# Performance work log

Measured on AMD Instinct MI355X. Metric: run time of the kernel, lower is better.

Reference implementation:

```python
import jax, jax.numpy as jnp
import numpy as np

D = 1024
HID = D // 2          # 512
HLEN = 15
IN_DIM = 4
B, N = 32, 512
EPS = 1e-5


def setup_inputs() -> dict:
    key = jax.random.key(0)
    ks = jax.random.split(key, 16)
    inp = {
        "tokens": jax.random.normal(ks[0], (B, N, D), dtype=jnp.float32),
        "history_traj": jax.random.normal(ks[1], (B, N, HLEN, IN_DIM), dtype=jnp.float32),
        "history_abs": jax.random.normal(ks[2], (B, N, 2), dtype=jnp.float32),
        "ego_speed": jax.random.uniform(ks[3], (B,), dtype=jnp.float32),
        "gps_confidence": jax.random.uniform(ks[4], (B,), dtype=jnp.float32),
        # LSTM params (PyTorch layout: gates stacked i,f,g,o along dim 0)
        "W_ih": jax.random.normal(ks[5], (4 * HID, IN_DIM), dtype=jnp.float32) * (1.0 / np.sqrt(IN_DIM)),
        "W_hh": jax.random.normal(ks[6], (4 * HID, HID), dtype=jnp.float32) * (1.0 / np.sqrt(HID)),
        "b_ih": jnp.zeros((4 * HID,), dtype=jnp.float32),
        "b_hh": jnp.zeros((4 * HID,), dtype=jnp.float32),
        "W_rel": jax.random.normal(ks[7], (D, HID), dtype=jnp.float32) * (0.1 / np.sqrt(HID)),
        "W_abs": jax.random.normal(ks[8], (D, 2), dtype=jnp.float32) * 0.1,
        "W_g1": jax.random.normal(ks[9], (16, 2), dtype=jnp.float32) * 0.5,
        "b_g1": jnp.zeros((16,), dtype=jnp.float32),
        "W_g2": jax.random.normal(ks[10], (1, 16), dtype=jnp.float32) * 0.25,
        "b_g2": jnp.zeros((1,), dtype=jnp.float32),
        "gamma": jnp.ones((D,), dtype=jnp.float32),
        "beta": jnp.zeros((D,), dtype=jnp.float32),
    }
    return inp


def _lstm_final_hidden(x, W_ih, W_hh, b_ih, b_hh):
    """x: (BN, H, in) -> final hidden state (BN, HID). PyTorch gate order i,f,g,o."""
    BN = x.shape[0]
    # precompute input contribution for all steps: (H, BN, 4*HID)
    xg = jnp.einsum('bhi,gi->hbg', x, W_ih) + (b_ih + b_hh)

    def step(carry, xg_t):
        h, c = carry
        gates = xg_t + h @ W_hh.T  # (BN, 4*HID)
        i, f, g, o = jnp.split(gates, 4, axis=-1)
        i = jax.nn.sigmoid(i)
        f = jax.nn.sigmoid(f)
        g = jnp.tanh(g)
        o = jax.nn.sigmoid(o)
        c = f * c + i * g
        h = o * jnp.tanh(c)
        return (h, c), None

    h0 = jnp.zeros((BN, HID), dtype=x.dtype)
    c0 = jnp.zeros((BN, HID), dtype=x.dtype)
    (h, _), _ = jax.lax.scan(step, (h0, c0), xg)
    return h


def reference(tokens, history_traj, history_abs, ego_speed, gps_confidence,
              W_ih, W_hh, b_ih, b_hh, W_rel, W_abs, W_g1, b_g1, W_g2, b_g2,
              gamma, beta):
    Bv, Nv, Dv = tokens.shape
    Hv = history_traj.shape[2]
    traj_flat = history_traj.reshape(Bv * Nv, Hv, -1)
    h_n = _lstm_final_hidden(traj_flat, W_ih, W_hh, b_ih, b_hh)  # (B*N, HID)
    h_rel = (h_n @ W_rel.T).reshape(Bv, Nv, Dv)                  # (B, N, D)
    h_abs = history_abs @ W_abs.T                                # (B, N, D)
    conf = jnp.stack([ego_speed, gps_confidence], axis=-1)       # (B, 2)
    gate = jax.nn.relu(conf @ W_g1.T + b_g1) @ W_g2.T + b_g2     # (B, 1)
    alpha = jax.nn.sigmoid(gate)[:, None, :]                     # (B, 1, 1)
    h_fused = alpha * h_rel + (1.0 - alpha) * h_abs
    x = tokens + h_fused
    mu = jnp.mean(x, axis=-1, keepdims=True)
    var = jnp.mean(jnp.square(x - mu), axis=-1, keepdims=True)
    return (x - mu) * jax.lax.rsqrt(var + EPS) * gamma + beta
```

## Files before the change

kernel.cpp:

```cpp
#include <hip/hip_runtime.h>
#include <hip/hip_bf16.h>
#include <math.h>

#define BB 32
#define NN 512
#define BN 16384
#define DD 1024
#define HID 512
#define G4 2048
#define HLEN 15
#define IND 4
#define EPS 1e-5f

typedef __bf16 v8bf __attribute__((ext_vector_type(8)));
typedef float  v4f  __attribute__((ext_vector_type(4)));

__device__ __forceinline__ void async_copy16(const __bf16* gsrc, __bf16* ldst) {
    __builtin_amdgcn_global_load_lds(
        (const __attribute__((address_space(1))) void*)gsrc,
        (__attribute__((address_space(3))) void*)ldst, 16, 0, 0);
}

#define VMCNTI(n) asm volatile("s_waitcnt vmcnt(" #n ")" ::: "memory")
#define VMCNT4 VMCNTI(4)
#define VMCNT0 VMCNTI(0)
#define LGKM0  asm volatile("s_waitcnt lgkmcnt(0)" ::: "memory")
#define MEMFENCE asm volatile("" ::: "memory")

#define LOG2E 1.44269504f
__device__ __forceinline__ float sigmf(float x) {
    return __builtin_amdgcn_rcpf(1.0f + __builtin_amdgcn_exp2f(-LOG2E * x));
}
__device__ __forceinline__ float tanh_fast(float x) {
    return 1.0f - 2.0f * __builtin_amdgcn_rcpf(1.0f + __builtin_amdgcn_exp2f(2.0f * LOG2E * x));
}

__global__ void convert_w(const float* __restrict__ Whh, const float* __restrict__ Wrel,
                          const float* __restrict__ Wih, const float* __restrict__ bih,
                          const float* __restrict__ bhh,
                          __bf16* __restrict__ whh_b, __bf16* __restrict__ wrel_b,
                          float* __restrict__ wih_i, float* __restrict__ bsum) {
    int i = blockIdx.x * 256 + threadIdx.x;
    if (i < G4 * HID) whh_b[i] = (__bf16)Whh[i];
    if (i < DD * HID) wrel_b[i] = (__bf16)Wrel[i];
    if (i < G4) {
        int uu = i >> 2, gi = i & 3;
        int src = gi * HID + uu;
        wih_i[i * 4 + 0] = Wih[src * 4 + 0];
        wih_i[i * 4 + 1] = Wih[src * 4 + 1];
        wih_i[i * 4 + 2] = Wih[src * 4 + 2];
        wih_i[i * 4 + 3] = Wih[src * 4 + 3];
        bsum[i] = bih[src] + bhh[src];
    }
}

__global__ void alpha_kernel(const float* __restrict__ es, const float* __restrict__ gc,
                             const float* __restrict__ W_g1, const float* __restrict__ b_g1,
                             const float* __restrict__ W_g2, const float* __restrict__ b_g2,
                             float* __restrict__ alpha) {
    int b = threadIdx.x;
    if (b >= BB) return;
    float c0 = es[b], c1 = gc[b];
    float acc = b_g2[0];
    for (int k = 0; k < 16; ++k) {
        float hk = c0 * W_g1[k * 2] + c1 * W_g1[k * 2 + 1] + b_g1[k];
        hk = fmaxf(hk, 0.0f);
        acc += hk * W_g2[k];
    }
    alpha[b] = 1.0f / (1.0f + expf(-acc));
}

__global__ __launch_bounds__(256) void lstm_cell0(const float* __restrict__ traj,
                                                  const float* __restrict__ wih_i,
                                                  const float* __restrict__ bsum,
                                                  float* __restrict__ c,
                                                  __bf16* __restrict__ h) {
    int idx = blockIdx.x * 256 + threadIdx.x;
    int row = idx >> 9;
    float4 x = *(const float4*)(traj + (size_t)row * (HLEN * IND));
    int u = idx & 511;
    float g[4];
    #pragma unroll
    for (int gi = 0; gi < 4; ++gi) {
        int j = u * 4 + gi;
        float4 w = *(const float4*)(wih_i + (size_t)j * 4);
        g[gi] = bsum[j] + w.x * x.x + w.y * x.y + w.z * x.z + w.w * x.w;
    }
    float ig = sigmf(g[0]);
    float gg = tanh_fast(g[2]);
    float og = sigmf(g[3]);
    float cn = ig * gg;
    c[idx] = cn;
    h[idx] = (__bf16)(og * tanh_fast(cn));
}


__device__ __forceinline__ void bar_acq() {
    __builtin_amdgcn_s_barrier();
    LGKM0;
    __builtin_amdgcn_sched_barrier(0);
}
__device__ __forceinline__ void bar_rel() {
    __builtin_amdgcn_s_barrier();
    MEMFENCE;
}

template<int IG, int GH, bool RA, bool RB>
__device__ __forceinline__ void phase_read(const __bf16* smb, int wave_m, int wn,
                                           int mrow, int pcs,
                                           v8bf (&ar)[4][2], v8bf (&br)[2][2][2]) {
    if (RA) {
        #pragma unroll
        for (int ii = 0; ii < 4; ++ii)
            #pragma unroll
            for (int ks = 0; ks < 2; ++ks)
                ar[ii][ks] = *(const v8bf*)(smb +
                    (wave_m * 128 + IG * 64 + ii * 16 + mrow) * 64 + ks * 32 + pcs);
    }
    if (RB) {
        #pragma unroll
        for (int g2 = 0; g2 < 2; ++g2)
            #pragma unroll
            for (int ks = 0; ks < 2; ++ks)
                br[GH][g2][ks] = *(const v8bf*)(smb + 16384 +
                    ((GH * 2 + g2) * 64 + wn * 16 + mrow) * 64 + ks * 32 + pcs);
    }
}

template<int IG, int GH>
__device__ __forceinline__ void phase_mfma(v8bf (&ar)[4][2], v8bf (&br)[2][2][2],
                                           v4f (&acc)[8][4]) {
    __builtin_amdgcn_s_setprio(1);
    #pragma unroll
    for (int ii = 0; ii < 4; ++ii)
        #pragma unroll
        for (int g2 = 0; g2 < 2; ++g2)
            #pragma unroll
            for (int ks = 0; ks < 2; ++ks)
                acc[IG * 4 + ii][GH * 2 + g2] = __builtin_amdgcn_mfma_f32_16x16x32_bf16(
                    ar[ii][ks], br[GH][g2][ks], acc[IG * 4 + ii][GH * 2 + g2], 0, 0, 0);
    __builtin_amdgcn_s_setprio(0);
}

__global__ __launch_bounds__(512, 2) void gemm_lstm(const __bf16* __restrict__ A,
                                                    const __bf16* __restrict__ Bm,
                                                    const float* __restrict__ traj,
                                                    const float* __restrict__ wih_i,
                                                    const float* __restrict__ bsum,
                                                    float* __restrict__ c,
                                                    __bf16* __restrict__ h_out,
                                                    int t) {
    __shared__ __bf16 sm[2][32768];

    const int tid    = threadIdx.x;
    const int lane   = tid & 63;
    const int wave   = tid >> 6;
    const int wave_m = wave & 1;
    const int wn     = wave >> 1;
    const int bm     = blockIdx.x;
    const int ub     = blockIdx.y;

    const int mrow = lane & 15;
    const int pcs  = (((lane >> 4) ^ ((mrow >> 2) & 3)) << 3);

    const __bf16* pa[4];
    const __bf16* pb[4];
    #pragma unroll
    for (int s = 0; s < 4; ++s) {
        const int ca = tid + s * 512;
        const int r  = ca >> 3, p = ca & 7;
        const int sl = p >> 2, l2 = (p & 3) ^ ((r >> 2) & 3);
        pa[s] = A + (size_t)(bm * 256 + r) * HID + sl * 32 + l2 * 8;
        const int g = r >> 6, ul = r & 63;
        pb[s] = Bm + (size_t)(g * HID + ub * 64 + ul) * HID + sl * 32 + l2 * 8;
    }
    const int wb = wave * 512;

    #define STAGE_A(buf, kt) do {                                        \
        async_copy16(pa[0] + (kt) * 64, &sm[buf][wb]);                   \
        async_copy16(pa[1] + (kt) * 64, &sm[buf][wb + 4096]);            \
        async_copy16(pa[2] + (kt) * 64, &sm[buf][wb + 8192]);            \
        async_copy16(pa[3] + (kt) * 64, &sm[buf][wb + 12288]); } while (0)
    #define STAGE_BLO(buf, kt) do {                                      \
        async_copy16(pb[0] + (kt) * 64, &sm[buf][16384 + wb]);           \
        async_copy16(pb[1] + (kt) * 64, &sm[buf][16384 + wb + 4096]); } while (0)
    #define STAGE_BHI(buf, kt) do {                                      \
        async_copy16(pb[2] + (kt) * 64, &sm[buf][16384 + wb + 8192]);    \
        async_copy16(pb[3] + (kt) * 64, &sm[buf][16384 + wb + 12288]); } while (0)

    v4f  acc[8][4] = {};
    v8bf ar[4][2];
    v8bf br[2][2][2];

    STAGE_A(0, 0); STAGE_BLO(0, 0); STAGE_BHI(0, 0);
    VMCNTI(2);
    __builtin_amdgcn_s_barrier();
    MEMFENCE;

    #pragma unroll
    for (int kt = 0; kt < 7; ++kt) {
        const int cb = kt & 1, nb = cb ^ 1;
        const __bf16* smb = &sm[cb][0];
        phase_read<0, 0, true, true>(smb, wave_m, wn, mrow, pcs, ar, br);
        if (nb) { STAGE_A(1, kt + 1); } else { STAGE_A(0, kt + 1); }
        bar_acq();  phase_mfma<0, 0>(ar, br, acc);  bar_rel();
        phase_read<1, 0, true, false>(smb, wave_m, wn, mrow, pcs, ar, br);
        if (nb) { STAGE_BLO(1, kt + 1); } else { STAGE_BLO(0, kt + 1); }
        VMCNTI(6);
        bar_acq();  phase_mfma<1, 0>(ar, br, acc);  bar_rel();
        phase_read<1, 1, false, true>(smb, wave_m, wn, mrow, pcs, ar, br);
        if (nb) { STAGE_BHI(1, kt + 1); } else { STAGE_BHI(0, kt + 1); }
        bar_acq();  phase_mfma<1, 1>(ar, br, acc);  bar_rel();
        phase_read<0, 1, true, false>(smb, wave_m, wn, mrow, pcs, ar, br);
        VMCNTI(2);
        bar_acq();  phase_mfma<0, 1>(ar, br, acc);  bar_rel();
    }

    VMCNT0;
    __builtin_amdgcn_s_barrier();
    MEMFENCE;
    {
        const __bf16* smb = &sm[1][0];
        phase_read<0, 0, true, true >(smb, wave_m, wn, mrow, pcs, ar, br);
        LGKM0; __builtin_amdgcn_sched_barrier(0);  phase_mfma<0, 0>(ar, br, acc);
        phase_read<1, 0, true, false>(smb, wave_m, wn, mrow, pcs, ar, br);
        LGKM0; __builtin_amdgcn_sched_barrier(0);  phase_mfma<1, 0>(ar, br, acc);
        phase_read<1, 1, false, true>(smb, wave_m, wn, mrow, pcs, ar, br);
        LGKM0; __builtin_amdgcn_sched_barrier(0);  phase_mfma<1, 1>(ar, br, acc);
        phase_read<0, 1, true, false>(smb, wave_m, wn, mrow, pcs, ar, br);
        LGKM0; __builtin_amdgcn_sched_barrier(0);  phase_mfma<0, 1>(ar, br, acc);
    }
    #undef STAGE_A
    #undef STAGE_BLO
    #undef STAGE_BHI

    const int u_glob = ub * 64 + wn * 16 + mrow;
    const int crow4  = (lane >> 4) * 4;
    float wv[4][4], bs4[4];
    #pragma unroll
    for (int gi = 0; gi < 4; ++gi) {
        float4 wp = *(const float4*)(wih_i + (size_t)(u_glob * 4 + gi) * 4);
        wv[gi][0] = wp.x; wv[gi][1] = wp.y; wv[gi][2] = wp.z; wv[gi][3] = wp.w;
        bs4[gi] = bsum[u_glob * 4 + gi];
    }
    #pragma unroll
    for (int i = 0; i < 8; ++i) {
        const int growb = bm * 256 + wave_m * 128 + (i >> 2) * 64 + (i & 3) * 16 + crow4;
        #pragma unroll
        for (int r = 0; r < 4; ++r) {
            const int grow = growb + r;
            const float4 x = *(const float4*)(traj + (size_t)grow * (HLEN * IND) + t * IND);
            float g[4];
            #pragma unroll
            for (int gi = 0; gi < 4; ++gi)
                g[gi] = acc[i][gi][r] + bs4[gi]
                      + wv[gi][0] * x.x + wv[gi][1] * x.y + wv[gi][2] * x.z + wv[gi][3] * x.w;
            float ig = sigmf(g[0]);
            float fg = sigmf(g[1]);
            float gg = tanh_fast(g[2]);
            float og = sigmf(g[3]);
            size_t ci = (size_t)grow * HID + u_glob;
            float cn = fg * c[ci] + ig * gg;
            c[ci] = cn;
            h_out[ci] = (__bf16)(og * tanh_fast(cn));
        }
    }
}

__global__ __launch_bounds__(256) void gemm_proj(const __bf16* __restrict__ A,
                                                 const __bf16* __restrict__ Bm,
                                                 __bf16* __restrict__ Cout) {
    __shared__ __bf16 sA[3][128][32];
    __shared__ __bf16 sB[3][128][32];
    const int K = HID, Nn = DD;
    const int tid  = threadIdx.x;
    const int lane = tid & 63;
    const int wave = tid >> 6;
    const int wm = (wave & 1) * 64;
    const int wn = (wave >> 1) * 64;
    const int bm = blockIdx.x;
    const int bn = blockIdx.y;

    v4f acc[4][4] = {};

    const int srow   = tid >> 2;
    const int schunk = (tid & 3) ^ ((srow >> 1) & 3);

    const __bf16* gA = A  + (size_t)(bm * 128 + srow) * K + schunk * 8;
    const __bf16* gB = Bm + (size_t)(bn * 128 + srow) * K + schunk * 8;
    __bf16* lA = &sA[0][0][0] + wave * 512;
    __bf16* lB = &sB[0][0][0] + wave * 512;

    const int mrow = lane & 15;
    const int pc   = ((lane >> 4) ^ ((mrow >> 1) & 3)) * 8;

    #define STAGE(buf, kt)                                        \
        do {                                                      \
            const __bf16* pA_ = gA + (kt) * 32;                   \
            const __bf16* pB_ = gB + (kt) * 32;                   \
            __bf16* dA_ = lA + (buf) * 4096;                      \
            __bf16* dB_ = lB + (buf) * 4096;                      \
            async_copy16(pA_,          dA_);                      \
            async_copy16(pA_ + 64 * K, dA_ + 2048);               \
            async_copy16(pB_,          dB_);                      \
            async_copy16(pB_ + 64 * K, dB_ + 2048);               \
        } while (0)

    STAGE(0, 0);
    STAGE(1, 1);
    #pragma unroll
    for (int k = 0; k < 16; ++k) {
        if (k < 15) { VMCNT4; } else { VMCNT0; }
        __builtin_amdgcn_s_barrier();
        MEMFENCE;
        if (k + 2 < 16) STAGE((k + 2) % 3, k + 2);
        const int cur = k % 3;
        v8bf af[4], bfr[4];
        #pragma unroll
        for (int i = 0; i < 4; ++i) af[i]  = *(v8bf*)&sA[cur][wm + i * 16 + mrow][pc];
        #pragma unroll
        for (int j = 0; j < 4; ++j) bfr[j] = *(v8bf*)&sB[cur][wn + j * 16 + mrow][pc];
        #pragma unroll
        for (int i = 0; i < 4; ++i)
            #pragma unroll
            for (int j = 0; j < 4; ++j)
                acc[i][j] = __builtin_amdgcn_mfma_f32_16x16x32_bf16(af[i], bfr[j], acc[i][j], 0, 0, 0);
    }
    #undef STAGE

    const int ccol  = lane & 15;
    const int crow4 = (lane >> 4) * 4;
    #pragma unroll
    for (int i = 0; i < 4; ++i)
        #pragma unroll
        for (int j = 0; j < 4; ++j) {
            int gm = bm * 128 + wm + i * 16 + crow4;
            int gn = bn * 128 + wn + j * 16 + ccol;
            #pragma unroll
            for (int r = 0; r < 4; ++r)
                Cout[(size_t)(gm + r) * Nn + gn] = (__bf16)acc[i][j][r];
        }
}

__global__ __launch_bounds__(256) void fuse_ln(const float* __restrict__ tokens,
                                               const __bf16* __restrict__ hrel,
                                               const float* __restrict__ habs_in,
                                               const float* __restrict__ W_abs,
                                               const float* __restrict__ alpha,
                                               const float* __restrict__ gamma,
                                               const float* __restrict__ beta,
                                               float* __restrict__ out) {
    const int row = blockIdx.x;
    const int b   = row >> 9;
    const float al = alpha[b];
    const float a0 = habs_in[(size_t)row * 2];
    const float a1 = habs_in[(size_t)row * 2 + 1];
    const int tid  = threadIdx.x;
    const int lane = tid & 63;
    const int wave = tid >> 6;

    __shared__ float red[4];

    float x[4];
    float s = 0.0f;
    #pragma unroll
    for (int q = 0; q < 4; ++q) {
        int dcol = tid + q * 256;
        float habs = a0 * W_abs[dcol * 2] + a1 * W_abs[dcol * 2 + 1];
        float v = tokens[(size_t)row * DD + dcol]
                + al * (float)hrel[(size_t)row * DD + dcol]
                + (1.0f - al) * habs;
        x[q] = v;
        s += v;
    }
    #pragma unroll
    for (int off = 32; off > 0; off >>= 1) s += __shfl_down(s, off);
    if (lane == 0) red[wave] = s;
    __syncthreads();
    float mu = (red[0] + red[1] + red[2] + red[3]) * (1.0f / DD);

    float vs = 0.0f;
    #pragma unroll
    for (int q = 0; q < 4; ++q) {
        float d = x[q] - mu;
        vs += d * d;
    }
    #pragma unroll
    for (int off = 32; off > 0; off >>= 1) vs += __shfl_down(vs, off);
    __syncthreads();
    if (lane == 0) red[wave] = vs;
    __syncthreads();
    float var = (red[0] + red[1] + red[2] + red[3]) * (1.0f / DD);
    float rstd = rsqrtf(var + EPS);

    #pragma unroll
    for (int q = 0; q < 4; ++q) {
        int dcol = tid + q * 256;
        out[(size_t)row * DD + dcol] = (x[q] - mu) * rstd * gamma[dcol] + beta[dcol];
    }
}

extern "C" void kernel_launch(void* const* d_in, const int* in_sizes, int n_in,
                              void* d_out, int out_size, void* d_ws, size_t ws_size,
                              hipStream_t stream) {
    const float* tokens   = (const float*)d_in[0];
    const float* traj     = (const float*)d_in[1];
    const float* habs     = (const float*)d_in[2];
    const float* espeed   = (const float*)d_in[3];
    const float* gconf    = (const float*)d_in[4];
    const float* W_ih     = (const float*)d_in[5];
    const float* W_hh     = (const float*)d_in[6];
    const float* b_ih     = (const float*)d_in[7];
    const float* b_hh     = (const float*)d_in[8];
    const float* W_rel    = (const float*)d_in[9];
    const float* W_abs    = (const float*)d_in[10];
    const float* W_g1     = (const float*)d_in[11];
    const float* b_g1     = (const float*)d_in[12];
    const float* W_g2     = (const float*)d_in[13];
    const float* b_g2     = (const float*)d_in[14];
    const float* gamma    = (const float*)d_in[15];
    const float* beta     = (const float*)d_in[16];
    float* out = (float*)d_out;

    char* ws = (char*)d_ws;
    size_t off = 0;
    __bf16* whh_b  = (__bf16*)(ws + off); off += (size_t)G4 * HID * 2;
    __bf16* wrel_b = (__bf16*)(ws + off); off += (size_t)DD * HID * 2;
    float*  wih_i  = (float*)(ws + off);  off += (size_t)G4 * 4 * 4;
    float*  bsum   = (float*)(ws + off);  off += (size_t)G4 * 4;
    __bf16* h0     = (__bf16*)(ws + off); off += (size_t)BN * HID * 2;
    __bf16* h1     = (__bf16*)(ws + off); off += (size_t)BN * HID * 2;
    float*  c      = (float*)(ws + off);  off += (size_t)BN * HID * 4;
    __bf16* hrel   = (__bf16*)(ws + off); off += (size_t)BN * DD * 2;
    float*  alpha  = (float*)(ws + off);  off += 256;

    convert_w<<<(G4 * HID + 255) / 256, 256, 0, stream>>>(W_hh, W_rel, W_ih, b_ih, b_hh,
                                                          whh_b, wrel_b, wih_i, bsum);
    alpha_kernel<<<1, 64, 0, stream>>>(espeed, gconf, W_g1, b_g1, W_g2, b_g2, alpha);
    lstm_cell0<<<(BN * HID) / 256, 256, 0, stream>>>(traj, wih_i, bsum, c, h0);

    __bf16* hbuf[2] = {h0, h1};
    for (int t = 1; t < HLEN; ++t) {
        const __bf16* hin = hbuf[(t + 1) & 1];
        __bf16* hout = hbuf[t & 1];
        gemm_lstm<<<dim3(BN / 256, HID / 64), 512, 0, stream>>>(hin, whh_b, traj, wih_i, bsum,
                                                                c, hout, t);
    }
    gemm_proj<<<dim3(BN / 128, DD / 128), 256, 0, stream>>>(h0, wrel_b, hrel);
    fuse_ln<<<BN, 256, 0, stream>>>(tokens, hrel, habs, W_abs, alpha, gamma, beta, out);
}
```

Before: 1.057 ms.

## Reuse 256x256 pipelined GEMM body for projection and widen LDS XOR swizzle

Moves the 256-tile, 8-wave, double-buffered phased MFMA GEMM body into a shared macro and uses it for the output projection as well, replacing the smaller 128x128 three-stage kernel. It also changes the LDS swizzle from a 2-bit to a 3-bit XOR across the 64-element row, aiming to cut LDS bank conflicts in both GEMMs. The larger projection tile improves operand reuse but leaves only 256 blocks, and the swizzle change has to stay consistent between the staging addresses and the fragment reads.

Result: faster. 868.3 us (-17.9%).

```diff
diff --git a/kernel.cpp b/kernel.cpp
--- a/kernel.cpp
+++ b/kernel.cpp
@@ -22,7 +22,6 @@
 }
 
 #define VMCNTI(n) asm volatile("s_waitcnt vmcnt(" #n ")" ::: "memory")
-#define VMCNT4 VMCNTI(4)
 #define VMCNT0 VMCNTI(0)
 #define LGKM0  asm volatile("s_waitcnt lgkmcnt(0)" ::: "memory")
 #define MEMFENCE asm volatile("" ::: "memory")
@@ -115,7 +114,7 @@
             #pragma unroll
             for (int ks = 0; ks < 2; ++ks)
                 ar[ii][ks] = *(const v8bf*)(smb +
-                    (wave_m * 128 + IG * 64 + ii * 16 + mrow) * 64 + ks * 32 + pcs);
+                    (wave_m * 128 + IG * 64 + ii * 16 + mrow) * 64 + ((ks * 32) ^ pcs));
     }
     if (RB) {
         #pragma unroll
@@ -123,7 +122,7 @@
             #pragma unroll
             for (int ks = 0; ks < 2; ++ks)
                 br[GH][g2][ks] = *(const v8bf*)(smb + 16384 +
-                    ((GH * 2 + g2) * 64 + wn * 16 + mrow) * 64 + ks * 32 + pcs);
+                    ((GH * 2 + g2) * 64 + wn * 16 + mrow) * 64 + ((ks * 32) ^ pcs));
     }
 }
 
@@ -141,6 +140,59 @@
                     ar[ii][ks], br[GH][g2][ks], acc[IG * 4 + ii][GH * 2 + g2], 0, 0, 0);
     __builtin_amdgcn_s_setprio(0);
 }
+
+#define STAGE_A(buf, kt) do {                                        \
+    async_copy16(pa[0] + (kt) * 64, &sm[buf][wb]);                   \
+    async_copy16(pa[1] + (kt) * 64, &sm[buf][wb + 4096]);            \
+    async_copy16(pa[2] + (kt) * 64, &sm[buf][wb + 8192]);            \
+    async_copy16(pa[3] + (kt) * 64, &sm[buf][wb + 12288]); } while (0)
+#define STAGE_BLO(buf, kt) do {                                      \
+    async_copy16(pb[0] + (kt) * 64, &sm[buf][16384 + wb]);           \
+    async_copy16(pb[1] + (kt) * 64, &sm[buf][16384 + wb + 4096]); } while (0)
+#define STAGE_BHI(buf, kt) do {                                      \
+    async_copy16(pb[2] + (kt) * 64, &sm[buf][16384 + wb + 8192]);    \
+    async_copy16(pb[3] + (kt) * 64, &sm[buf][16384 + wb + 12288]); } while (0)
+
+#define GEMM256_BODY                                                               \
+    v4f  acc[8][4] = {};                                                           \
+    v8bf ar[4][2];                                                                 \
+    v8bf br[2][2][2];                                                              \
+    STAGE_A(0, 0); STAGE_BLO(0, 0); STAGE_BHI(0, 0);                               \
+    VMCNTI(2);                                                                     \
+    __builtin_amdgcn_s_barrier();                                                  \
+    MEMFENCE;                                                                      \
+    _Pragma("unroll")                                                              \
+    for (int kt = 0; kt < 7; ++kt) {                                               \
+        const int nb = (kt & 1) ^ 1;                                               \
+        const __bf16* smb = &sm[kt & 1][0];                                        \
+        phase_read<0, 0, true, true>(smb, wave_m, wn, mrow, pcs, ar, br);          \
+        if (nb) { STAGE_A(1, kt + 1); } else { STAGE_A(0, kt + 1); }               \
+        bar_acq();  phase_mfma<0, 0>(ar, br, acc);  bar_rel();                     \
+        phase_read<1, 0, true, false>(smb, wave_m, wn, mrow, pcs, ar, br);         \
+        if (nb) { STAGE_BLO(1, kt + 1); } else { STAGE_BLO(0, kt + 1); }           \
+        VMCNTI(6);                                                                 \
+        bar_acq();  phase_mfma<1, 0>(ar, br, acc);  bar_rel();                     \
+        phase_read<1, 1, false, true>(smb, wave_m, wn, mrow, pcs, ar, br);         \
+        if (nb) { STAGE_BHI(1, kt + 1); } else { STAGE_BHI(0, kt + 1); }           \
+        bar_acq();  phase_mfma<1, 1>(ar, br, acc);  bar_rel();                     \
+        phase_read<0, 1, true, false>(smb, wave_m, wn, mrow, pcs, ar, br);         \
+        VMCNTI(2);                                                                 \
+        bar_acq();  phase_mfma<0, 1>(ar, br, acc);  bar_rel();                     \
+    }                                                                              \
+    VMCNT0;                                                                        \
+    __builtin_amdgcn_s_barrier();                                                  \
+    MEMFENCE;                                                                      \
+    {                                                                              \
+        const __bf16* smb = &sm[1][0];                                             \
+        phase_read<0, 0, true, true >(smb, wave_m, wn, mrow, pcs, ar, br);         \
+        LGKM0; __builtin_amdgcn_sched_barrier(0);  phase_mfma<0, 0>(ar, br, acc);  \
+        phase_read<1, 0, true, false>(smb, wave_m, wn, mrow, pcs, ar, br);         \
+        LGKM0; __builtin_amdgcn_sched_barrier(0);  phase_mfma<1, 0>(ar, br, acc);  \
+        phase_read<1, 1, false, true>(smb, wave_m, wn, mrow, pcs, ar, br);         \
+        LGKM0; __builtin_amdgcn_sched_barrier(0);  phase_mfma<1, 1>(ar, br, acc);  \
+        phase_read<0, 1, true, false>(smb, wave_m, wn, mrow, pcs, ar, br);         \
+        LGKM0; __builtin_amdgcn_sched_barrier(0);  phase_mfma<0, 1>(ar, br, acc);  \
+    }
 
 __global__ __launch_bounds__(512, 2) void gemm_lstm(const __bf16* __restrict__ A,
                                                     const __bf16* __restrict__ Bm,
@@ -161,78 +213,22 @@
     const int ub     = blockIdx.y;
 
     const int mrow = lane & 15;
-    const int pcs  = (((lane >> 4) ^ ((mrow >> 2) & 3)) << 3);
+    const int pcs  = (((lane >> 4) ^ (mrow & 7)) << 3);
 
     const __bf16* pa[4];
     const __bf16* pb[4];
     #pragma unroll
     for (int s = 0; s < 4; ++s) {
         const int ca = tid + s * 512;
-        const int r  = ca >> 3, p = ca & 7;
-        const int sl = p >> 2, l2 = (p & 3) ^ ((r >> 2) & 3);
-        pa[s] = A + (size_t)(bm * 256 + r) * HID + sl * 32 + l2 * 8;
+        const int r  = ca >> 3;
+        const int l  = (ca & 7) ^ (r & 7);
+        pa[s] = A + (size_t)(bm * 256 + r) * HID + l * 8;
         const int g = r >> 6, ul = r & 63;
-        pb[s] = Bm + (size_t)(g * HID + ub * 64 + ul) * HID + sl * 32 + l2 * 8;
+        pb[s] = Bm + (size_t)(g * HID + ub * 64 + ul) * HID + l * 8;
     }
     const int wb = wave * 512;
 
-    #define STAGE_A(buf, kt) do {                                        \
-        async_copy16(pa[0] + (kt) * 64, &sm[buf][wb]);                   \
-        async_copy16(pa[1] + (kt) * 64, &sm[buf][wb + 4096]);            \
-        async_copy16(pa[2] + (kt) * 64, &sm[buf][wb + 8192]);            \
-        async_copy16(pa[3] + (kt) * 64, &sm[buf][wb + 12288]); } while (0)
-    #define STAGE_BLO(buf, kt) do {                                      \
-        async_copy16(pb[0] + (kt) * 64, &sm[buf][16384 + wb]);           \
-        async_copy16(pb[1] + (kt) * 64, &sm[buf][16384 + wb + 4096]); } while (0)
-    #define STAGE_BHI(buf, kt) do {                                      \
-        async_copy16(pb[2] + (kt) * 64, &sm[buf][16384 + wb + 8192]);    \
-        async_copy16(pb[3] + (kt) * 64, &sm[buf][16384 + wb + 12288]); } while (0)
-
-    v4f  acc[8][4] = {};
-    v8bf ar[4][2];
-    v8bf br[2][2][2];
-
-    STAGE_A(0, 0); STAGE_BLO(0, 0); STAGE_BHI(0, 0);
-    VMCNTI(2);
-    __builtin_amdgcn_s_barrier();
-    MEMFENCE;
-
-    #pragma unroll
-    for (int kt = 0; kt < 7; ++kt) {
-        const int cb = kt & 1, nb = cb ^ 1;
-        const __bf16* smb = &sm[cb][0];
-        phase_read<0, 0, true, true>(smb, wave_m, wn, mrow, pcs, ar, br);
-        if (nb) { STAGE_A(1, kt + 1); } else { STAGE_A(0, kt + 1); }
-        bar_acq();  phase_mfma<0, 0>(ar, br, acc);  bar_rel();
-        phase_read<1, 0, true, false>(smb, wave_m, wn, mrow, pcs, ar, br);
-        if (nb) { STAGE_BLO(1, kt + 1); } else { STAGE_BLO(0, kt + 1); }
-        VMCNTI(6);
-        bar_acq();  phase_mfma<1, 0>(ar, br, acc);  bar_rel();
-        phase_read<1, 1, false, true>(smb, wave_m, wn, mrow, pcs, ar, br);
-        if (nb) { STAGE_BHI(1, kt + 1); } else { STAGE_BHI(0, kt + 1); }
-        bar_acq();  phase_mfma<1, 1>(ar, br, acc);  bar_rel();
-        phase_read<0, 1, true, false>(smb, wave_m, wn, mrow, pcs, ar, br);
-        VMCNTI(2);
-        bar_acq();  phase_mfma<0, 1>(ar, br, acc);  bar_rel();
-    }
-
-    VMCNT0;
-    __builtin_amdgcn_s_barrier();
-    MEMFENCE;
-    {
-        const __bf16* smb = &sm[1][0];
-        phase_read<0, 0, true, true >(smb, wave_m, wn, mrow, pcs, ar, br);
-        LGKM0; __builtin_amdgcn_sched_barrier(0);  phase_mfma<0, 0>(ar, br, acc);
-        phase_read<1, 0, true, false>(smb, wave_m, wn, mrow, pcs, ar, br);
-        LGKM0; __builtin_amdgcn_sched_barrier(0);  phase_mfma<1, 0>(ar, br, acc);
-        phase_read<1, 1, false, true>(smb, wave_m, wn, mrow, pcs, ar, br);
-        LGKM0; __builtin_amdgcn_sched_barrier(0);  phase_mfma<1, 1>(ar, br, acc);
-        phase_read<0, 1, true, false>(smb, wave_m, wn, mrow, pcs, ar, br);
-        LGKM0; __builtin_amdgcn_sched_barrier(0);  phase_mfma<0, 1>(ar, br, acc);
-    }
-    #undef STAGE_A
-    #undef STAGE_BLO
-    #undef STAGE_BHI
+    GEMM256_BODY
 
     const int u_glob = ub * 64 + wn * 16 + mrow;
     const int crow4  = (lane >> 4) * 4;
@@ -267,79 +263,48 @@
     }
 }
 
-__global__ __launch_bounds__(256) void gemm_proj(const __bf16* __restrict__ A,
-                                                 const __bf16* __restrict__ Bm,
-                                                 __bf16* __restrict__ Cout) {
-    __shared__ __bf16 sA[3][128][32];
-    __shared__ __bf16 sB[3][128][32];
-    const int K = HID, Nn = DD;
-    const int tid  = threadIdx.x;
-    const int lane = tid & 63;
-    const int wave = tid >> 6;
-    const int wm = (wave & 1) * 64;
-    const int wn = (wave >> 1) * 64;
-    const int bm = blockIdx.x;
-    const int bn = blockIdx.y;
-
-    v4f acc[4][4] = {};
-
-    const int srow   = tid >> 2;
-    const int schunk = (tid & 3) ^ ((srow >> 1) & 3);
-
-    const __bf16* gA = A  + (size_t)(bm * 128 + srow) * K + schunk * 8;
-    const __bf16* gB = Bm + (size_t)(bn * 128 + srow) * K + schunk * 8;
-    __bf16* lA = &sA[0][0][0] + wave * 512;
-    __bf16* lB = &sB[0][0][0] + wave * 512;
+__global__ __launch_bounds__(512, 2) void gemm_proj(const __bf16* __restrict__ A,
+                                                    const __bf16* __restrict__ Bm,
+                                                    __bf16* __restrict__ Cout) {
+    __shared__ __bf16 sm[2][32768];
+
+    const int tid    = threadIdx.x;
+    const int lane   = tid & 63;
+    const int wave   = tid >> 6;
+    const int wave_m = wave & 1;
+    const int wn     = wave >> 1;
+    const int bm     = blockIdx.x;
+    const int bn     = blockIdx.y;
 
     const int mrow = lane & 15;
-    const int pc   = ((lane >> 4) ^ ((mrow >> 1) & 3)) * 8;
-
-    #define STAGE(buf, kt)                                        \
-        do {                                                      \
-            const __bf16* pA_ = gA + (kt) * 32;                   \
-            const __bf16* pB_ = gB + (kt) * 32;                   \
-            __bf16* dA_ = lA + (buf) * 4096;                      \
-            __bf16* dB_ = lB + (buf) * 4096;                      \
-            async_copy16(pA_,          dA_);                      \
-            async_copy16(pA_ + 64 * K, dA_ + 2048);               \
-            async_copy16(pB_,          dB_);                      \
-            async_copy16(pB_ + 64 * K, dB_ + 2048);               \
-        } while (0)
-
-    STAGE(0, 0);
-    STAGE(1, 1);
-    #pragma unroll
-    for (int k = 0; k < 16; ++k) {
-        if (k < 15) { VMCNT4; } else { VMCNT0; }
-        __builtin_amdgcn_s_barrier();
-        MEMFENCE;
-        if (k + 2 < 16) STAGE((k + 2) % 3, k + 2);
-        const int cur = k % 3;
-        v8bf af[4], bfr[4];
-        #pragma unroll
-        for (int i = 0; i < 4; ++i) af[i]  = *(v8bf*)&sA[cur][wm + i * 16 + mrow][pc];
-        #pragma unroll
-        for (int j = 0; j < 4; ++j) bfr[j] = *(v8bf*)&sB[cur][wn + j * 16 + mrow][pc];
-        #pragma unroll
-        for (int i = 0; i < 4; ++i)
-            #pragma unroll
-            for (int j = 0; j < 4; ++j)
-                acc[i][j] = __builtin_amdgcn_mfma_f32_16x16x32_bf16(af[i], bfr[j], acc[i][j], 0, 0, 0);
-    }
-    #undef STAGE
-
-    const int ccol  = lane & 15;
+    const int pcs  = (((lane >> 4) ^ (mrow & 7)) << 3);
+
+    const __bf16* pa[4];
+    const __bf16* pb[4];
+    #pragma unroll
+    for (int s = 0; s < 4; ++s) {
+        const int ca = tid + s * 512;
+        const int r  = ca >> 3;
+        const int l  = (ca & 7) ^ (r & 7);
+        pa[s] = A  + (size_t)(bm * 256 + r) * HID + l * 8;
+        pb[s] = Bm + (size_t)(bn * 256 + r) * HID + l * 8;
+    }
+    const int wb = wave * 512;
+
+    GEMM256_BODY
+
     const int crow4 = (lane >> 4) * 4;
     #pragma unroll
-    for (int i = 0; i < 4; ++i)
+    for (int i = 0; i < 8; ++i) {
+        const int growb = bm * 256 + wave_m * 128 + (i >> 2) * 64 + (i & 3) * 16 + crow4;
         #pragma unroll
         for (int j = 0; j < 4; ++j) {
-            int gm = bm * 128 + wm + i * 16 + crow4;
-            int gn = bn * 128 + wn + j * 16 + ccol;
+            const int gcol = bn * 256 + j * 64 + wn * 16 + mrow;
             #pragma unroll
             for (int r = 0; r < 4; ++r)
-                Cout[(size_t)(gm + r) * Nn + gn] = (__bf16)acc[i][j][r];
+                Cout[(size_t)(growb + r) * DD + gcol] = (__bf16)acc[i][j][r];
         }
+    }
 }
 
 __global__ __launch_bounds__(256) void fuse_ln(const float* __restrict__ tokens,
@@ -446,6 +411,6 @@
         gemm_lstm<<<dim3(BN / 256, HID / 64), 512, 0, stream>>>(hin, whh_b, traj, wih_i, bsum,
                                                                 c, hout, t);
     }
-    gemm_proj<<<dim3(BN / 128, DD / 128), 256, 0, stream>>>(h0, wrel_b, hrel);
+    gemm_proj<<<dim3(BN / 256, DD / 256), 512, 0, stream>>>(h0, wrel_b, hrel);
     fuse_ln<<<BN, 256, 0, stream>>>(tokens, hrel, habs, W_abs, alpha, gamma, beta, out);
 }
```
